# Kernel optimization log

Hardware: AMD Instinct MI355X
Metric: run time of the kernel (lower is better)

Reference implementation:

```python
import jax, jax.numpy as jnp
import numpy as np

B, S, D, H = 4096, 200, 128, 64


def setup_inputs() -> dict:
    key = jax.random.key(0)
    ks = jax.random.split(key, 8)
    X_series = jax.random.normal(ks[0], (B, S, D), dtype=jnp.float32)
    pos_series = jax.random.normal(ks[1], (S, D), dtype=jnp.float32)
    X_item = jax.random.normal(ks[2], (B, D), dtype=jnp.float32)
    valid_mask = jax.random.randint(ks[3], (B, S), 0, 2) > 0
    valid_mask = valid_mask.at[:, 0].set(True)  # avoid all-masked rows (NaN softmax)
    glorot = jax.nn.initializers.glorot_uniform()
    Wc = glorot(ks[4], (D, H), jnp.float32)
    Wp = glorot(ks[5], (D, H), jnp.float32)
    We = glorot(ks[6], (D, H), jnp.float32)
    z = jax.random.normal(ks[7], (H,), dtype=jnp.float32) * 0.1
    return {"X_series": X_series, "pos_series": pos_series, "X_item": X_item,
            "valid_mask": valid_mask, "Wc": Wc, "Wp": Wp, "We": We, "z": z}


def reference(X_series, pos_series, X_item, valid_mask, Wc, Wp, We, z):
    # additive attention pre-activation: [B,S,H]
    pre = (X_item @ Wc)[:, None, :] + X_series @ We + (pos_series @ Wp)[None, :, :]
    # scores: sum over hidden of z * tanh(pre) -> [B,S]
    scores = jnp.einsum('bsh,h->bs', jnp.tanh(pre), z)
    # raw masked score sum (pre-softmax), [B,1]
    score_sum = jnp.sum(jnp.where(valid_mask, scores, 0.0), axis=-1, keepdims=True)
    # masked softmax over seq
    attn = jax.nn.softmax(jnp.where(valid_mask, scores, -jnp.inf), axis=-1)
    # weighted sum over seq -> [B,D]
    attention_output = jnp.einsum('bs,bsd->bd', attn, X_series)
    return jnp.concatenate([attention_output, score_sum], axis=1)
```

## Files before the change

### kernel.cpp

```cpp
#include <hip/hip_runtime.h>

#define BB 4096
#define SS 200
#define DD 128
#define HH 64
#define NT 13
#define OUTW (DD + 1)

typedef __attribute__((ext_vector_type(4))) float f32x4;
typedef _Float16 f16x8 __attribute__((ext_vector_type(8)));

template <int CTRL>
__device__ __forceinline__ float dpp_add(float x) {
  int xi = __float_as_int(x);
  int yi = __builtin_amdgcn_update_dpp(xi, xi, CTRL, 0xF, 0xF, false);
  return x + __int_as_float(yi);
}
__device__ __forceinline__ float row16_sum(float x) {
  x = dpp_add<0xB1>(x);
  x = dpp_add<0x4E>(x);
  x = dpp_add<0x124>(x);
  x = dpp_add<0x128>(x);
  return x;
}

__global__ void setup_kernel(const float* __restrict__ pos,
                             const float* __restrict__ Wp,
                             const float* __restrict__ We,
                             const void* __restrict__ maskv,
                             const float* __restrict__ Xi,
                             const float* __restrict__ Wc,
                             float* __restrict__ Pmat,
                             _Float16* __restrict__ Bfrag,
                             float* __restrict__ cw,
                             int* __restrict__ flag) {
  __shared__ int anyf[4];
  const int blk = blockIdx.x;
  const int t = threadIdx.x;
  if (blk < SS) {
    if (t < HH) {
      float acc = 0.f;
      #pragma unroll 8
      for (int d = 0; d < DD; ++d) acc = fmaf(pos[blk * DD + d], Wp[d * HH + t], acc);
      Pmat[blk * HH + t] = acc;
    }
  } else if (blk == SS) {
    for (int id = t; id < 1024; id += 256) {
      int lane = id & 63;
      int kt = (id >> 6) & 3;
      int ct = id >> 8;
      int kbase = kt * 32 + 8 * (lane >> 4);
      int n = ct * 16 + (lane & 15);
      _Float16* dst = Bfrag + id * 8;
      #pragma unroll
      for (int j = 0; j < 8; ++j) dst[j] = (_Float16)We[(kbase + j) * HH + n];
    }
  } else if (blk == SS + 1) {
    const unsigned char* mb = (const unsigned char*)maskv;
    int local = 0;
    for (int i = t; i < 4096; i += 256)
      if ((i & 3) != 0 && mb[i] != 0) local = 1;
    unsigned long long bal = __ballot(local != 0);
    if ((t & 63) == 0) anyf[t >> 6] = (bal != 0ull) ? 1 : 0;
    __syncthreads();
    if (t == 0) *flag = (anyf[0] | anyf[1] | anyf[2] | anyf[3]);
  } else {
    const int w = t >> 6, lane = t & 63;
    const int base = (blk - (SS + 2)) * 8 + w * 2;
    const float* xi0 = Xi + (size_t)base * DD;
    const float* xi1 = xi0 + DD;
    const float* wc = Wc + lane;
    float a0 = 0.f, a1 = 0.f;
    #pragma unroll 8
    for (int d = 0; d < DD; ++d) {
      const float wv = wc[d * HH];
      a0 = fmaf(xi0[d], wv, a0);
      a1 = fmaf(xi1[d], wv, a1);
    }
    cw[(size_t)base * HH + lane] = a0;
    cw[(size_t)(base + 1) * HH + lane] = a1;
  }
}

__global__ void swizzle_kernel(const float* __restrict__ Pmat, _Float16* __restrict__ Psw) {
  const int tile = blockIdx.x;
  const int tid = threadIdx.x;
  const int half = tid >> 6, lane = tid & 63;
  _Float16* dst = Psw + ((size_t)(tile * 2 + half) * 64 + lane) * 8;
  #pragma unroll
  for (int e = 0; e < 8; ++e) {
    const int ct = (half << 1) | (e >> 2);
    const int r = e & 3;
    int s = tile * 16 + ((lane >> 4) << 2) + r;
    if (s >= SS) s = SS - 1;
    dst[e] = (_Float16)Pmat[s * HH + ct * 16 + (lane & 15)];
  }
}

__global__ __launch_bounds__(256, 2) void fused_kernel(
    const float* __restrict__ Xs, const void* __restrict__ maskv,
    const float* __restrict__ zv, const float* __restrict__ cw,
    const _Float16* __restrict__ Comb,
    const int* __restrict__ flagp,
    float* __restrict__ out) {
  __shared__ __align__(16) float xlds[4][2][2048];

  const int t = threadIdx.x;
  const int lane = t & 63;
  const int w = t >> 6;
  const int lg = lane >> 4;
  const int lr = lane & 15;
  const int b = blockIdx.x * 4 + w;

  const float* Xrow = Xs + (size_t)b * (SS * DD);
  const f16x8* pswb = (const f16x8*)(Comb + 8192);

  auto stage_tile = [&](int tt, int buf) {
    float* dst = &xlds[w][buf][0];
    #pragma unroll
    for (int k = 0; k < 8; ++k) {
      const int row = 2 * k + (lane >> 5);
      int grow = tt * 16 + row; if (grow >= SS) grow = SS - 1;
      const int c = (lane & 31) ^ row;
      const float* src = Xrow + (size_t)grow * DD + c * 4;
      __builtin_amdgcn_global_load_lds(
          (const __attribute__((address_space(1))) void*)src,
          (__attribute__((address_space(3))) void*)(dst + k * 256),
          16, 0, 0);
    }
  };

  stage_tile(0, 0);
  f16x8 pn0 = pswb[lane];
  f16x8 pn1 = pswb[64 + lane];

  f16x8 bfr[16];
  {
    const f16x8* bg = (const f16x8*)Comb;
    #pragma unroll
    for (int i = 0; i < 16; ++i) bfr[i] = bg[i * 64 + lane];
  }

  float c4[4], z4[4];
  #pragma unroll
  for (int ct = 0; ct < 4; ++ct) {
    c4[ct] = cw[(size_t)b * HH + ct * 16 + lr];
    z4[ct] = zv[ct * 16 + lr];
  }

  const int mflag = *flagp;
  unsigned mbits = 0;
  if (mflag) {
    const unsigned char* mbp = (const unsigned char*)maskv + (size_t)b * SS;
    #pragma unroll
    for (int tt = 0; tt < NT; ++tt) {
      const int srow = tt * 16 + lr;
      unsigned v = (srow < SS) ? (unsigned)mbp[srow] : 0u;
      mbits |= (v ? 1u : 0u) << tt;
    }
  } else {
    const int* mip = (const int*)maskv + (size_t)b * SS;
    #pragma unroll
    for (int tt = 0; tt < NT; ++tt) {
      const int srow = tt * 16 + lr;
      unsigned v = (srow < SS) ? (unsigned)(mip[srow] != 0) : 0u;
      mbits |= v << tt;
    }
  }

  float part[4][8];
  #pragma unroll
  for (int kt = 0; kt < 4; ++kt)
    #pragma unroll
    for (int j = 0; j < 8; ++j) part[kt][j] = 0.f;
  float usum = 0.f, ssum = 0.f;
  int cur = 0;

  for (int tt = 0; tt < NT; ++tt) {
    asm volatile("s_waitcnt vmcnt(0)" ::: "memory");
    __builtin_amdgcn_sched_barrier(0);
    f32x4 acc[4];
    #pragma unroll
    for (int ct = 0; ct < 4; ++ct) {
      #pragma unroll
      for (int r = 0; r < 4; ++r) {
        const float pv = (ct < 2) ? (float)pn0[ct * 4 + r] : (float)pn1[(ct - 2) * 4 + r];
        acc[ct][r] = pv + c4[ct];
      }
    }
    if (tt + 1 < NT) {
      stage_tile(tt + 1, cur ^ 1);
      pn0 = pswb[(tt + 1) * 128 + lane];
      pn1 = pswb[(tt + 1) * 128 + 64 + lane];
    }
    const float* bufp = &xlds[w][cur][0];
    f16x8 af[4];
    #pragma unroll
    for (int kt = 0; kt < 4; ++kt) {
      const int ch = lg * 2 + kt * 8;
      const f32x4 v0 = *(const f32x4*)&bufp[lr * 128 + (((ch    ) ^ lr) * 4)];
      const f32x4 v1 = *(const f32x4*)&bufp[lr * 128 + (((ch + 1) ^ lr) * 4)];
      f16x8 v;
      v[0] = (_Float16)v0[0]; v[1] = (_Float16)v0[1];
      v[2] = (_Float16)v0[2]; v[3] = (_Float16)v0[3];
      v[4] = (_Float16)v1[0]; v[5] = (_Float16)v1[1];
      v[6] = (_Float16)v1[2]; v[7] = (_Float16)v1[3];
      af[kt] = v;
    }
    #pragma unroll
    for (int kt = 0; kt < 4; ++kt)
      #pragma unroll
      for (int ct = 0; ct < 4; ++ct)
        acc[ct] = __builtin_amdgcn_mfma_f32_16x16x32_f16(af[kt], bfr[ct * 4 + kt], acc[ct], 0, 0, 0);
    float sc[4];
    #pragma unroll
    for (int r = 0; r < 4; ++r) {
      float p = 0.f;
      #pragma unroll
      for (int ct = 0; ct < 4; ++ct) {
        const float e2 = __expf(2.f * acc[ct][r]);
        const float th = 1.f - 2.f * __builtin_amdgcn_rcpf(e2 + 1.f);
        p = fmaf(z4[ct], th, p);
      }
      sc[r] = row16_sum(p);
    }
    const float s01 = (lr & 1) ? sc[1] : sc[0];
    const float s23 = (lr & 1) ? sc[3] : sc[2];
    const float sel = (lr & 2) ? s23 : s01;
    const float mysc = __shfl(sel, ((lr >> 2) << 4) | lr, 64);
    const bool mv = (mbits >> tt) & 1u;
    const float u = mv ? __expf(mysc) : 0.f;
    ssum += mv ? mysc : 0.f;
    usum += u;
    #pragma unroll
    for (int kt = 0; kt < 4; ++kt)
      #pragma unroll
      for (int j = 0; j < 8; ++j)
        part[kt][j] = fmaf(u, (float)af[kt][j], part[kt][j]);
    cur ^= 1;
  }

  #pragma unroll
  for (int kt = 0; kt < 4; ++kt)
    #pragma unroll
    for (int j = 0; j < 8; ++j)
      part[kt][j] = row16_sum(part[kt][j]);
  usum = row16_sum(usum);
  ssum = row16_sum(ssum);

  const float inv = 1.f / usum;
  if (lr == 0) {
    float* ob = out + (size_t)b * OUTW;
    #pragma unroll
    for (int kt = 0; kt < 4; ++kt)
      #pragma unroll
      for (int j = 0; j < 8; ++j)
        ob[kt * 32 + lg * 8 + j] = part[kt][j] * inv;
  }
  if (lane == 8) out[(size_t)b * OUTW + DD] = ssum;
}

extern "C" void kernel_launch(void* const* d_in, const int* in_sizes, int n_in,
                              void* d_out, int out_size, void* d_ws, size_t ws_size,
                              hipStream_t stream) {
  const float* Xs  = (const float*)d_in[0];
  const float* pos = (const float*)d_in[1];
  const float* Xi  = (const float*)d_in[2];
  const void*  mk  = d_in[3];
  const float* Wc  = (const float*)d_in[4];
  const float* Wp  = (const float*)d_in[5];
  const float* We  = (const float*)d_in[6];
  const float* zv  = (const float*)d_in[7];
  float* out = (float*)d_out;

  char* ws = (char*)d_ws;
  int*      flag  = (int*)ws;
  float*    Pmat  = (float*)(ws + 256);
  _Float16* Bfrag = (_Float16*)(ws + 256 + SS * HH * 4);
  _Float16* Psw   = (_Float16*)(ws + 256 + SS * HH * 4 + 16384);
  float*    cw    = (float*)(ws + 94464);

  setup_kernel<<<SS + 2 + BB / 8, 256, 0, stream>>>(pos, Wp, We, mk, Xi, Wc,
                                                    Pmat, Bfrag, cw, flag);
  swizzle_kernel<<<NT, 128, 0, stream>>>(Pmat, Psw);
  fused_kernel<<<BB / 4, 256, 0, stream>>>(Xs, mk, zv, cw, Bfrag, flag, out);
}
```

Measured before the change: 95.44 us.

## Restructure setup kernels: fuse pos projection with swizzle, precompute mask bitmasks

```diff
diff --git a/kernel.cpp b/kernel.cpp
--- a/kernel.cpp
+++ b/kernel.cpp
@@ -24,27 +24,38 @@
   return x;
 }
 
-__global__ void setup_kernel(const float* __restrict__ pos,
-                             const float* __restrict__ Wp,
-                             const float* __restrict__ We,
-                             const void* __restrict__ maskv,
-                             const float* __restrict__ Xi,
-                             const float* __restrict__ Wc,
-                             float* __restrict__ Pmat,
-                             _Float16* __restrict__ Bfrag,
-                             float* __restrict__ cw,
-                             int* __restrict__ flag) {
+__global__ void setupA_kernel(const float* __restrict__ pos,
+                              const float* __restrict__ Wp,
+                              const float* __restrict__ We,
+                              const void* __restrict__ maskv,
+                              _Float16* __restrict__ Bfrag,
+                              _Float16* __restrict__ Psw,
+                              int* __restrict__ flag) {
   __shared__ int anyf[4];
   const int blk = blockIdx.x;
   const int t = threadIdx.x;
-  if (blk < SS) {
-    if (t < HH) {
-      float acc = 0.f;
+  if (blk < NT) {
+    const int tile = blk;
+    for (int id = t; id < 1024; id += 256) {
+      const int half = id >> 9;
+      const int lane = (id >> 3) & 63;
+      const int e = id & 7;
+      const int ct = (half << 1) | (e >> 2);
+      const int r = e & 3;
+      int s = tile * 16 + ((lane >> 4) << 2) + r;
+      if (s >= SS) s = SS - 1;
+      const int h = ct * 16 + (lane & 15);
+      const float* pr = pos + (size_t)s * DD;
+      const float* wp = Wp + h;
+      float a0 = 0.f, a1 = 0.f;
       #pragma unroll 8
-      for (int d = 0; d < DD; ++d) acc = fmaf(pos[blk * DD + d], Wp[d * HH + t], acc);
-      Pmat[blk * HH + t] = acc;
-    }
-  } else if (blk == SS) {
+      for (int d = 0; d < DD; d += 2) {
+        a0 = fmaf(pr[d], wp[d * HH], a0);
+        a1 = fmaf(pr[d + 1], wp[(d + 1) * HH], a1);
+      }
+      Psw[((size_t)(tile * 2 + half) * 64 + lane) * 8 + e] = (_Float16)(a0 + a1);
+    }
+  } else if (blk == NT) {
     for (int id = t; id < 1024; id += 256) {
       int lane = id & 63;
       int kt = (id >> 6) & 3;
@@ -55,7 +66,7 @@
       #pragma unroll
       for (int j = 0; j < 8; ++j) dst[j] = (_Float16)We[(kbase + j) * HH + n];
     }
-  } else if (blk == SS + 1) {
+  } else {
     const unsigned char* mb = (const unsigned char*)maskv;
     int local = 0;
     for (int i = t; i < 4096; i += 256)
@@ -64,10 +75,21 @@
     if ((t & 63) == 0) anyf[t >> 6] = (bal != 0ull) ? 1 : 0;
     __syncthreads();
     if (t == 0) *flag = (anyf[0] | anyf[1] | anyf[2] | anyf[3]);
-  } else {
-    const int w = t >> 6, lane = t & 63;
-    const int base = (blk - (SS + 2)) * 8 + w * 2;
-    const float* xi0 = Xi + (size_t)base * DD;
+  }
+}
+
+__global__ void setupB_kernel(const float* __restrict__ Xi,
+                              const float* __restrict__ Wc,
+                              const void* __restrict__ maskv,
+                              const int* __restrict__ flagp,
+                              float* __restrict__ cw,
+                              unsigned short* __restrict__ mbitsArr) {
+  const int t = threadIdx.x;
+  const int w = t >> 6, lane = t & 63;
+  const int base = blockIdx.x * 8;
+  {
+    const int b0 = base + w * 2;
+    const float* xi0 = Xi + (size_t)b0 * DD;
     const float* xi1 = xi0 + DD;
     const float* wc = Wc + lane;
     float a0 = 0.f, a1 = 0.f;
@@ -77,31 +99,40 @@
       a0 = fmaf(xi0[d], wv, a0);
       a1 = fmaf(xi1[d], wv, a1);
     }
-    cw[(size_t)base * HH + lane] = a0;
-    cw[(size_t)(base + 1) * HH + lane] = a1;
-  }
-}
-
-__global__ void swizzle_kernel(const float* __restrict__ Pmat, _Float16* __restrict__ Psw) {
-  const int tile = blockIdx.x;
-  const int tid = threadIdx.x;
-  const int half = tid >> 6, lane = tid & 63;
-  _Float16* dst = Psw + ((size_t)(tile * 2 + half) * 64 + lane) * 8;
-  #pragma unroll
-  for (int e = 0; e < 8; ++e) {
-    const int ct = (half << 1) | (e >> 2);
-    const int r = e & 3;
-    int s = tile * 16 + ((lane >> 4) << 2) + r;
-    if (s >= SS) s = SS - 1;
-    dst[e] = (_Float16)Pmat[s * HH + ct * 16 + (lane & 15)];
+    cw[(size_t)b0 * HH + lane] = a0;
+    cw[(size_t)(b0 + 1) * HH + lane] = a1;
+  }
+  if (t < 128) {
+    const int b = base + (t >> 4);
+    const int lr = t & 15;
+    const int mflag = *flagp;
+    unsigned mb = 0;
+    if (mflag) {
+      const unsigned char* mbp = (const unsigned char*)maskv + (size_t)b * SS;
+      #pragma unroll
+      for (int tt = 0; tt < NT; ++tt) {
+        const int srow = tt * 16 + lr;
+        unsigned v = (srow < SS) ? (unsigned)mbp[srow] : 0u;
+        mb |= (v ? 1u : 0u) << tt;
+      }
+    } else {
+      const int* mip = (const int*)maskv + (size_t)b * SS;
+      #pragma unroll
+      for (int tt = 0; tt < NT; ++tt) {
+        const int srow = tt * 16 + lr;
+        unsigned v = (srow < SS) ? (unsigned)(mip[srow] != 0) : 0u;
+        mb |= v << tt;
+      }
+    }
+    mbitsArr[(size_t)b * 16 + lr] = (unsigned short)mb;
   }
 }
 
 __global__ __launch_bounds__(256, 2) void fused_kernel(
-    const float* __restrict__ Xs, const void* __restrict__ maskv,
+    const float* __restrict__ Xs,
     const float* __restrict__ zv, const float* __restrict__ cw,
+    const unsigned short* __restrict__ mbitsArr,
     const _Float16* __restrict__ Comb,
-    const int* __restrict__ flagp,
     float* __restrict__ out) {
   __shared__ __align__(16) float xlds[4][2][2048];
 
@@ -147,26 +178,7 @@
     c4[ct] = cw[(size_t)b * HH + ct * 16 + lr];
     z4[ct] = zv[ct * 16 + lr];
   }
-
-  const int mflag = *flagp;
-  unsigned mbits = 0;
-  if (mflag) {
-    const unsigned char* mbp = (const unsigned char*)maskv + (size_t)b * SS;
-    #pragma unroll
-    for (int tt = 0; tt < NT; ++tt) {
-      const int srow = tt * 16 + lr;
-      unsigned v = (srow < SS) ? (unsigned)mbp[srow] : 0u;
-      mbits |= (v ? 1u : 0u) << tt;
-    }
-  } else {
-    const int* mip = (const int*)maskv + (size_t)b * SS;
-    #pragma unroll
-    for (int tt = 0; tt < NT; ++tt) {
-      const int srow = tt * 16 + lr;
-      unsigned v = (srow < SS) ? (unsigned)(mip[srow] != 0) : 0u;
-      mbits |= v << tt;
-    }
-  }
+  const unsigned mbits = mbitsArr[(size_t)b * 16 + lr];
 
   float part[4][8];
   #pragma unroll
@@ -274,14 +286,13 @@
   float* out = (float*)d_out;
 
   char* ws = (char*)d_ws;
-  int*      flag  = (int*)ws;
-  float*    Pmat  = (float*)(ws + 256);
-  _Float16* Bfrag = (_Float16*)(ws + 256 + SS * HH * 4);
-  _Float16* Psw   = (_Float16*)(ws + 256 + SS * HH * 4 + 16384);
-  float*    cw    = (float*)(ws + 94464);
-
-  setup_kernel<<<SS + 2 + BB / 8, 256, 0, stream>>>(pos, Wp, We, mk, Xi, Wc,
-                                                    Pmat, Bfrag, cw, flag);
-  swizzle_kernel<<<NT, 128, 0, stream>>>(Pmat, Psw);
-  fused_kernel<<<BB / 4, 256, 0, stream>>>(Xs, mk, zv, cw, Bfrag, flag, out);
-}
+  int*            flag  = (int*)ws;
+  _Float16*       Bfrag = (_Float16*)(ws + 256);
+  _Float16*       Psw   = (_Float16*)(ws + 256 + 16384);
+  float*          cw    = (float*)(ws + 43520);
+  unsigned short* mbA   = (unsigned short*)(ws + 43520 + (size_t)BB * HH * 4);
+
+  setupA_kernel<<<NT + 2, 256, 0, stream>>>(pos, Wp, We, mk, Bfrag, Psw, flag);
+  setupB_kernel<<<BB / 8, 256, 0, stream>>>(Xi, Wc, mk, flag, cw, mbA);
+  fused_kernel<<<BB / 4, 256, 0, stream>>>(Xs, zv, cw, mbA, Bfrag, out);
+}
```

Result: slower. 113.9 us (+19.4%).
